# Kernel optimization log

Measured on AMD Instinct MI355X. Metric: run time of the kernel, lower is better.

Reference implementation:

```python
import jax, jax.numpy as jnp
import numpy as np

N = 129  # fixed by fc1: 3*121 -> N-8 = 121
F = 262144
E = 16384

def setup_inputs() -> dict:
    key = jax.random.key(0)
    ks = jax.random.split(key, 18)
    s = 0.05
    return {
        "x": jax.random.normal(ks[0], (N, F), jnp.float32),
        "edge_index": jax.random.randint(ks[1], (2, E), 0, N),
        "edge_attr": jax.random.uniform(ks[2], (E, 3), jnp.float32),
        # GCNConvSortPool (channel1 only; forward reuses it for all 3 edge channels)
        "gcn1_W": jax.random.normal(ks[3], (F, 1), jnp.float32) * (1.0 / np.sqrt(F)),
        "gcn1_b": jnp.zeros((1,), jnp.float32),
        "gcn2_W": jax.random.normal(ks[4], (1, 1), jnp.float32),
        "gcn2_b": jnp.zeros((1,), jnp.float32),
        "conv1_w": jax.random.normal(ks[5], (3, 2, 3), jnp.float32) * s,  # OIH
        "conv1_b": jax.random.normal(ks[6], (3,), jnp.float32) * s,
        "conv2_w": jax.random.normal(ks[7], (1, 3, 3), jnp.float32) * s,
        "conv2_b": jax.random.normal(ks[8], (1,), jnp.float32) * s,
        "fc1_W": jax.random.normal(ks[9], (3 * 121, 32), jnp.float32) * s,
        "fc1_b": jnp.zeros((32,), jnp.float32),
        "fc2_W": jax.random.normal(ks[10], (32, 6), jnp.float32) * s,
        "fc2_b": jnp.zeros((6,), jnp.float32),
        "fc3_W": jax.random.normal(ks[11], (6, 2), jnp.float32) * s,
        "fc3_b": jnp.zeros((2,), jnp.float32),
    }

def _gcn_conv(x, row, col, ew, W, b):
    # PyG GCNConv with edge weights: add self loops (weight 1), symmetric norm.
    n = x.shape[0]
    xw = x @ W                                             # [n, out]
    loop = jnp.arange(n)
    row2 = jnp.concatenate([row, loop])
    col2 = jnp.concatenate([col, loop])
    ew2 = jnp.concatenate([ew, jnp.ones((n,), x.dtype)])
    deg = jax.ops.segment_sum(ew2, col2, num_segments=n)
    dinv = jnp.where(deg > 0, deg ** -0.5, 0.0)
    norm = dinv[row2] * ew2 * dinv[col2]                   # [e+n]
    out = jax.ops.segment_sum(norm[:, None] * xw[row2], col2, num_segments=n)
    return out + b

def _maxpool1d3(z):
    return jax.lax.reduce_window(z, -jnp.inf, jax.lax.max, (1, 1, 3), (1, 1, 1), 'VALID')

def _conv1d(z, w, b):
    out = jax.lax.conv_general_dilated(z, w, (1,), 'VALID', dimension_numbers=('NCH', 'OIH', 'NCH'))
    return out + b[None, :, None]

def _channel(x, row, col, ew, gcn1_W, gcn1_b, gcn2_W, gcn2_b, conv1_w, conv1_b, conv2_w, conv2_b):
    h1 = _gcn_conv(x, row, col, ew, gcn1_W, gcn1_b)        # [N,1]
    h2 = _gcn_conv(h1[:, -1:], row, col, ew, gcn2_W, gcn2_b)  # [N,1]
    h = jnp.concatenate([h1, h2], axis=-1)                 # [N,2]
    perm = jnp.argsort(-h[:, -1])                          # SortPool: sort by last channel, descending, k=N
    h = h[perm]                                            # [N,2]
    z = h.T[None]                                          # [1,2,N]
    z = _maxpool1d3(_conv1d(z, conv1_w, conv1_b))          # [1,3,N-4]
    z = _maxpool1d3(_conv1d(z, conv2_w, conv2_b))          # [1,1,N-8]
    return z

def reference(x, edge_index, edge_attr, gcn1_W, gcn1_b, gcn2_W, gcn2_b,
              conv1_w, conv1_b, conv2_w, conv2_b,
              fc1_W, fc1_b, fc2_W, fc2_b, fc3_W, fc3_b):
    row, col = edge_index[0], edge_index[1]
    outs = [_channel(x, row, col, edge_attr[:, c], gcn1_W, gcn1_b, gcn2_W, gcn2_b,
                     conv1_w, conv1_b, conv2_w, conv2_b) for c in range(3)]
    all_x = jnp.concatenate(outs, axis=-2)                 # [1,3,121]
    h = all_x.reshape(1, -1)                               # [1,363]
    h = jax.nn.elu(h @ fc1_W + fc1_b)                      # dropout=0 -> identity
    h = jax.nn.elu(h @ fc2_W + fc2_b)
    return h @ fc3_W + fc3_b                               # [1,2]
```

## Files before the change

kernel.cpp:

```cpp
#include <hip/hip_runtime.h>
#include <hip/hip_bf16.h>
#include <math.h>

#define NN 129
#define FF 262144
#define EE 16384
#define CHUNKS 32
#define CHUNK (FF / CHUNKS)
#define NMV (NN * CHUNKS)

#define EPT_T (EE / 256)
#define BATCH 8
#define NBATCH (EPT_T / BATCH)

#define OFF_PARTIAL 0
#define OFF_BAR     (OFF_PARTIAL + NMV)
#define LSTRIDE 32

typedef float vfloat4 __attribute__((ext_vector_type(4)));

__global__ __launch_bounds__(256) void k_fused(
    const float* __restrict__ x, const float* __restrict__ W,
    const int* __restrict__ eidx, const float* __restrict__ eattr,
    double* __restrict__ ws,
    const float* __restrict__ b1, const float* __restrict__ W2, const float* __restrict__ b2,
    const float* __restrict__ c1w, const float* __restrict__ c1b,
    const float* __restrict__ c2w, const float* __restrict__ c2b,
    const float* __restrict__ f1W, const float* __restrict__ f1b,
    const float* __restrict__ f2W, const float* __restrict__ f2b,
    const float* __restrict__ f3W, const float* __restrict__ f3b,
    float* __restrict__ out)
{
    const int b = blockIdx.x;
    const int tid = threadIdx.x;
    const int wave = tid >> 6, lane = tid & 63;

    __shared__ double P[129 + 387 + 387];
    __shared__ double SCR[1935];
    __shared__ double ws4[4];
    __shared__ double fcb[38];

    unsigned* sync = (unsigned*)(ws + OFF_BAR);

    if (b != 0) {
        const int bm = b - 1;
        const int r = bm / CHUNKS, ch = bm % CHUNKS;
        const vfloat4* xp = (const vfloat4*)(x + (size_t)r * FF + (size_t)ch * CHUNK);
        const float4*  wp = (const float4*)(W + (size_t)ch * CHUNK);
        double acc0 = 0.0, acc1 = 0.0;
#pragma unroll
        for (int i = 0; i < CHUNK / (256 * 4); ++i) {
            vfloat4 xv = __builtin_nontemporal_load(xp + tid + i * 256);
            float4  wv = wp[tid + i * 256];
            acc0 += (double)xv[0] * (double)wv.x + (double)xv[1] * (double)wv.y;
            acc1 += (double)xv[2] * (double)wv.z + (double)xv[3] * (double)wv.w;
        }
        double acc = acc0 + acc1;
        for (int off = 32; off > 0; off >>= 1) acc += __shfl_down(acc, off, 64);
        if (lane == 0) ws4[wave] = acc;
        __syncthreads();
        if (tid == 0) {
            const double v = (ws4[0] + ws4[1]) + (ws4[2] + ws4[3]);
            __hip_atomic_store(&ws[OFF_PARTIAL + bm], v,
                               __ATOMIC_RELAXED, __HIP_MEMORY_SCOPE_AGENT);
            asm volatile("s_waitcnt vmcnt(0)" ::: "memory");
            __hip_atomic_fetch_add(&sync[(bm & 63) * LSTRIDE], 1u,
                                   __ATOMIC_RELAXED, __HIP_MEMORY_SCOPE_AGENT);
        }
        return;
    }

    double* sxw   = P;
    double* sdinv = P + 129;
    double* sh1   = P + 516;
    double (*hp)[3][NN] = (double(*)[3][NN])SCR;

    for (int i = tid; i < 4 * 3 * NN; i += 256) ((double*)hp)[i] = 0.0;
    __syncthreads();
    for (int bt = 0; bt < NBATCH; ++bt) {
        int   c8[BATCH];
        float a8[BATCH][3];
#pragma unroll
        for (int i = 0; i < BATCH; ++i) {
            const int e = (bt * BATCH + i) * 256 + tid;
            c8[i] = eidx[EE + e];
            a8[i][0] = eattr[e * 3 + 0];
            a8[i][1] = eattr[e * 3 + 1];
            a8[i][2] = eattr[e * 3 + 2];
        }
#pragma unroll
        for (int i = 0; i < BATCH; ++i)
#pragma unroll
            for (int c = 0; c < 3; ++c)
                unsafeAtomicAdd(&hp[wave][c][c8[i]], (double)a8[i][c]);
    }
    __syncthreads();
    for (int v = tid; v < 3 * NN; v += 256) {
        const double d = 1.0 + (hp[0][0][0 ? 0 : 0], 0.0);
        (void)d;
    }
    for (int v = tid; v < 3 * NN; v += 256) {
        const int c = v / NN, j = v % NN;
        const double d = 1.0 + ((hp[0][c][j] + hp[1][c][j]) + (hp[2][c][j] + hp[3][c][j]));
        sdinv[v] = (d > 0.0) ? 1.0 / sqrt(d) : 0.0;
    }
    __syncthreads();

    if (tid < 64) {
        unsigned* c = sync + tid * LSTRIDE;
        const unsigned expct = (tid < 32) ? 65u : 64u;
        while (__hip_atomic_load(c, __ATOMIC_RELAXED, __HIP_MEMORY_SCOPE_AGENT) < expct)
            __builtin_amdgcn_s_sleep(8);
    }
    __syncthreads();

    for (int j = tid; j < NN; j += 256) {
        double s = 0.0;
#pragma unroll
        for (int k = 0; k < CHUNKS; ++k)
            s += __hip_atomic_load(&ws[OFF_PARTIAL + j * CHUNKS + k],
                                   __ATOMIC_RELAXED, __HIP_MEMORY_SCOPE_AGENT);
        sxw[j] = s;
    }
    for (int i = tid; i < 4 * 3 * NN; i += 256) ((double*)hp)[i] = 0.0;
    __syncthreads();

    for (int bt = 0; bt < NBATCH; ++bt) {
        int   r8[BATCH], c8[BATCH];
        float a8[BATCH][3];
#pragma unroll
        for (int i = 0; i < BATCH; ++i) {
            const int e = (bt * BATCH + i) * 256 + tid;
            r8[i] = eidx[e];
            c8[i] = eidx[EE + e];
            a8[i][0] = eattr[e * 3 + 0];
            a8[i][1] = eattr[e * 3 + 1];
            a8[i][2] = eattr[e * 3 + 2];
        }
#pragma unroll
        for (int i = 0; i < BATCH; ++i) {
            const int r = r8[i], cl = c8[i];
            const double xwr = sxw[r];
#pragma unroll
            for (int c = 0; c < 3; ++c) {
                const double nw = sdinv[c * NN + r] * (double)a8[i][c] * sdinv[c * NN + cl];
                unsafeAtomicAdd(&hp[wave][c][cl], nw * xwr);
            }
        }
    }
    __syncthreads();

    const double bb1 = (double)b1[0];
    for (int i = tid; i < 3 * NN; i += 256) {
        const int c = i / NN, j = i % NN;
        const double dv = sdinv[i];
        sh1[i] = dv * dv * sxw[j] + bb1 +
                 ((hp[0][c][j] + hp[1][c][j]) + (hp[2][c][j] + hp[3][c][j]));
    }
    __syncthreads();
    for (int i = tid; i < 4 * 3 * NN; i += 256) ((double*)hp)[i] = 0.0;
    __syncthreads();

    const double w2 = (double)W2[0];
    for (int bt = 0; bt < NBATCH; ++bt) {
        int   r8[BATCH], c8[BATCH];
        float a8[BATCH][3];
#pragma unroll
        for (int i = 0; i < BATCH; ++i) {
            const int e = (bt * BATCH + i) * 256 + tid;
            r8[i] = eidx[e];
            c8[i] = eidx[EE + e];
            a8[i][0] = eattr[e * 3 + 0];
            a8[i][1] = eattr[e * 3 + 1];
            a8[i][2] = eattr[e * 3 + 2];
        }
#pragma unroll
        for (int i = 0; i < BATCH; ++i) {
            const int r = r8[i], cl = c8[i];
#pragma unroll
            for (int c = 0; c < 3; ++c) {
                const double nw = sdinv[c * NN + r] * (double)a8[i][c] * sdinv[c * NN + cl];
                unsafeAtomicAdd(&hp[wave][c][cl], nw * (sh1[c * NN + r] * w2));
            }
        }
    }
    __syncthreads();

    double* h2f  = SCR + 1548;
    const double bb2 = (double)b2[0];
    for (int i = tid; i < 3 * NN; i += 256) {
        const int c = i / NN, j = i % NN;
        const double dv = sdinv[i];
        h2f[i] = dv * dv * (sh1[i] * w2) + bb2 +
                 ((hp[0][c][j] + hp[1][c][j]) + (hp[2][c][j] + hp[3][c][j]));
    }
    __syncthreads();

    double* z0   = SCR;
    double* z1   = SCR + 387;
    int*    rnk  = (int*)(SCR + 774);
    double* c1o  = SCR + 774;
    double* c2o  = SCR;
    double* allx = SCR + 369;
    double* fc1o = fcb;
    double* fc2o = fcb + 32;

    for (int i = tid; i < 3 * NN; i += 256) {
        const int c = i / NN, j = i % NN;
        const double v = h2f[c * NN + j];
        int rk = 0;
        for (int q = 0; q < NN; ++q) {
            const double u = h2f[c * NN + q];
            rk += (u > v) || (u == v && q < j);
        }
        rnk[i] = rk;
    }
    __syncthreads();
    for (int i = tid; i < 3 * NN; i += 256) {
        const int c = i / NN;
        const int rk = rnk[i];
        z0[c * NN + rk] = sh1[i];
        z1[c * NN + rk] = h2f[i];
    }
    __syncthreads();

    for (int i = tid; i < 3 * 3 * 127; i += 256) {
        const int c = i / (3 * 127), rem = i % (3 * 127), o = rem / 127, p = rem % 127;
        double s = (double)c1b[o];
#pragma unroll
        for (int k = 0; k < 3; ++k) {
            s += (double)c1w[(o * 2 + 0) * 3 + k] * z0[c * NN + p + k];
            s += (double)c1w[(o * 2 + 1) * 3 + k] * z1[c * NN + p + k];
        }
        c1o[(c * 3 + o) * 127 + p] = s;
    }
    __syncthreads();

    for (int i = tid; i < 3 * 123; i += 256) {
        const int c = i / 123, p = i % 123;
        double s = (double)c2b[0];
#pragma unroll
        for (int ic = 0; ic < 3; ++ic)
#pragma unroll
            for (int k = 0; k < 3; ++k) {
                const double* base = c1o + (c * 3 + ic) * 127 + p + k;
                const double m = fmax(base[0], fmax(base[1], base[2]));
                s += (double)c2w[ic * 3 + k] * m;
            }
        c2o[c * 123 + p] = s;
    }
    __syncthreads();
    for (int i = tid; i < 3 * 121; i += 256) {
        const int c = i / 121, p = i % 121;
        allx[c * 121 + p] = fmax(c2o[c * 123 + p],
                            fmax(c2o[c * 123 + p + 1], c2o[c * 123 + p + 2]));
    }
    __syncthreads();

    {
        const int j = tid >> 3, t = tid & 7;
        double s = 0.0;
        for (int i = t; i < 363; i += 8) s += allx[i] * (double)f1W[i * 32 + j];
        s += __shfl_down(s, 4, 8);
        s += __shfl_down(s, 2, 8);
        s += __shfl_down(s, 1, 8);
        if (t == 0) {
            s += (double)f1b[j];
            fc1o[j] = (s > 0.0) ? s : expm1(s);
        }
    }
    __syncthreads();
    if (tid < 6) {
        double s = (double)f2b[tid];
        for (int i = 0; i < 32; ++i) s += fc1o[i] * (double)f2W[i * 6 + tid];
        fc2o[tid] = (s > 0.0) ? s : expm1(s);
    }
    __syncthreads();
    if (tid < 2) {
        double s = (double)f3b[tid];
        for (int i = 0; i < 6; ++i) s += fc2o[i] * (double)f3W[i * 2 + tid];
        out[tid] = (float)s;
    }
}

extern "C" void kernel_launch(void* const* d_in, const int* in_sizes, int n_in,
                              void* d_out, int out_size, void* d_ws, size_t ws_size,
                              hipStream_t stream) {
    const float* x    = (const float*)d_in[0];
    const int*   eidx = (const int*)d_in[1];
    const float* eattr= (const float*)d_in[2];
    const float* g1W  = (const float*)d_in[3];
    const float* g1b  = (const float*)d_in[4];
    const float* g2W  = (const float*)d_in[5];
    const float* g2b  = (const float*)d_in[6];
    const float* c1w  = (const float*)d_in[7];
    const float* c1b  = (const float*)d_in[8];
    const float* c2w  = (const float*)d_in[9];
    const float* c2b  = (const float*)d_in[10];
    const float* f1W  = (const float*)d_in[11];
    const float* f1b  = (const float*)d_in[12];
    const float* f2W  = (const float*)d_in[13];
    const float* f2b  = (const float*)d_in[14];
    const float* f3W  = (const float*)d_in[15];
    const float* f3b  = (const float*)d_in[16];
    float* out = (float*)d_out;
    double* ws = (double*)d_ws;

    hipMemsetAsync((void*)(ws + OFF_BAR), 0, 64 * 128, stream);
    k_fused<<<NMV + 1, 256, 0, stream>>>(
        x, g1W, eidx, eattr, ws,
        g1b, g2W, g2b, c1w, c1b, c2w, c2b,
        f1W, f1b, f2W, f2b, f3W, f3b, out);
}
```

Before: 286.0 us.

## Counting-sort edges by destination and aggregate with run-length segmented sums

Block 0 now counting-sorts all edges by destination node into a global record buffer (packed row/col plus three attributes as float4). It then does the degree and both GCN aggregations by scanning contiguous per-thread runs and issuing one LDS atomic per run instead of one per edge per channel. The intent is to cut heavy shared-memory double-atomic contention in the single serial block. The cost is an extra global scatter and read-back pass and a serial prefix scan on one thread. Edge order within a bin is nondeterministic, so floating-point summation order can vary between runs.

```diff
diff --git a/kernel.cpp b/kernel.cpp
--- a/kernel.cpp
+++ b/kernel.cpp
@@ -15,6 +15,7 @@
 
 #define OFF_PARTIAL 0
 #define OFF_BAR     (OFF_PARTIAL + NMV)
+#define OFF_SORT    (OFF_BAR + 1024)
 #define LSTRIDE 32
 
 typedef float vfloat4 __attribute__((ext_vector_type(4)));
@@ -37,6 +38,8 @@
 
     __shared__ double P[129 + 387 + 387];
     __shared__ double SCR[1935];
+    __shared__ int    sbin[NN];
+    __shared__ int    scur[NN];
     __shared__ double ws4[4];
     __shared__ double fcb[38];
 
@@ -73,60 +76,27 @@
     double* sxw   = P;
     double* sdinv = P + 129;
     double* sh1   = P + 516;
-    double (*hp)[3][NN] = (double(*)[3][NN])SCR;
-
-    for (int i = tid; i < 4 * 3 * NN; i += 256) ((double*)hp)[i] = 0.0;
+    double* agg   = SCR;
+    float4* recs  = (float4*)(ws + OFF_SORT);
+
+    for (int i = tid; i < NN; i += 256) sbin[i] = 0;
     __syncthreads();
     for (int bt = 0; bt < NBATCH; ++bt) {
-        int   c8[BATCH];
-        float a8[BATCH][3];
-#pragma unroll
-        for (int i = 0; i < BATCH; ++i) {
-            const int e = (bt * BATCH + i) * 256 + tid;
-            c8[i] = eidx[EE + e];
-            a8[i][0] = eattr[e * 3 + 0];
-            a8[i][1] = eattr[e * 3 + 1];
-            a8[i][2] = eattr[e * 3 + 2];
-        }
+        int c8[BATCH];
 #pragma unroll
         for (int i = 0; i < BATCH; ++i)
-#pragma unroll
-            for (int c = 0; c < 3; ++c)
-                unsafeAtomicAdd(&hp[wave][c][c8[i]], (double)a8[i][c]);
-    }
-    __syncthreads();
-    for (int v = tid; v < 3 * NN; v += 256) {
-        const double d = 1.0 + (hp[0][0][0 ? 0 : 0], 0.0);
-        (void)d;
-    }
-    for (int v = tid; v < 3 * NN; v += 256) {
-        const int c = v / NN, j = v % NN;
-        const double d = 1.0 + ((hp[0][c][j] + hp[1][c][j]) + (hp[2][c][j] + hp[3][c][j]));
-        sdinv[v] = (d > 0.0) ? 1.0 / sqrt(d) : 0.0;
-    }
-    __syncthreads();
-
-    if (tid < 64) {
-        unsigned* c = sync + tid * LSTRIDE;
-        const unsigned expct = (tid < 32) ? 65u : 64u;
-        while (__hip_atomic_load(c, __ATOMIC_RELAXED, __HIP_MEMORY_SCOPE_AGENT) < expct)
-            __builtin_amdgcn_s_sleep(8);
-    }
-    __syncthreads();
-
-    for (int j = tid; j < NN; j += 256) {
-        double s = 0.0;
-#pragma unroll
-        for (int k = 0; k < CHUNKS; ++k)
-            s += __hip_atomic_load(&ws[OFF_PARTIAL + j * CHUNKS + k],
-                                   __ATOMIC_RELAXED, __HIP_MEMORY_SCOPE_AGENT);
-        sxw[j] = s;
-    }
-    for (int i = tid; i < 4 * 3 * NN; i += 256) ((double*)hp)[i] = 0.0;
-    __syncthreads();
-
+            c8[i] = eidx[EE + (bt * BATCH + i) * 256 + tid];
+#pragma unroll
+        for (int i = 0; i < BATCH; ++i) atomicAdd(&sbin[c8[i]], 1);
+    }
+    __syncthreads();
+    if (tid == 0) {
+        int run = 0;
+        for (int j = 0; j < NN; ++j) { scur[j] = run; run += sbin[j]; }
+    }
+    __syncthreads();
     for (int bt = 0; bt < NBATCH; ++bt) {
-        int   r8[BATCH], c8[BATCH];
+        int r8[BATCH], c8[BATCH];
         float a8[BATCH][3];
 #pragma unroll
         for (int i = 0; i < BATCH; ++i) {
@@ -139,60 +109,149 @@
         }
 #pragma unroll
         for (int i = 0; i < BATCH; ++i) {
-            const int r = r8[i], cl = c8[i];
+            const int pos = atomicAdd(&scur[c8[i]], 1);
+            float4 rec;
+            rec.x = __int_as_float((r8[i] << 8) | c8[i]);
+            rec.y = a8[i][0]; rec.z = a8[i][1]; rec.w = a8[i][2];
+            recs[pos] = rec;
+        }
+    }
+    __threadfence_block();
+    __syncthreads();
+
+    for (int i = tid; i < 3 * NN; i += 256) agg[i] = 0.0;
+    __syncthreads();
+    {
+        const int base = tid * EPT_T;
+        double a0 = 0.0, a1 = 0.0, a2 = 0.0;
+        int cur = -1;
+#pragma unroll 4
+        for (int k = 0; k < EPT_T; ++k) {
+            const float4 rec = recs[base + k];
+            const int rc = __float_as_int(rec.x);
+            const int cl = rc & 255;
+            if (cl != cur) {
+                if (cur >= 0) {
+                    unsafeAtomicAdd(&agg[0 * NN + cur], a0);
+                    unsafeAtomicAdd(&agg[1 * NN + cur], a1);
+                    unsafeAtomicAdd(&agg[2 * NN + cur], a2);
+                }
+                cur = cl; a0 = a1 = a2 = 0.0;
+            }
+            a0 += (double)rec.y; a1 += (double)rec.z; a2 += (double)rec.w;
+        }
+        if (cur >= 0) {
+            unsafeAtomicAdd(&agg[0 * NN + cur], a0);
+            unsafeAtomicAdd(&agg[1 * NN + cur], a1);
+            unsafeAtomicAdd(&agg[2 * NN + cur], a2);
+        }
+    }
+    __syncthreads();
+    for (int v = tid; v < 3 * NN; v += 256) {
+        const double d = 1.0 + agg[v];
+        sdinv[v] = (d > 0.0) ? 1.0 / sqrt(d) : 0.0;
+    }
+    __syncthreads();
+
+    if (tid < 64) {
+        unsigned* c = sync + tid * LSTRIDE;
+        const unsigned expct = (tid < 32) ? 65u : 64u;
+        while (__hip_atomic_load(c, __ATOMIC_RELAXED, __HIP_MEMORY_SCOPE_AGENT) < expct)
+            __builtin_amdgcn_s_sleep(8);
+    }
+    __syncthreads();
+
+    for (int j = tid; j < NN; j += 256) {
+        double s = 0.0;
+#pragma unroll
+        for (int k = 0; k < CHUNKS; ++k)
+            s += __hip_atomic_load(&ws[OFF_PARTIAL + j * CHUNKS + k],
+                                   __ATOMIC_RELAXED, __HIP_MEMORY_SCOPE_AGENT);
+        sxw[j] = s;
+    }
+    for (int i = tid; i < 3 * NN; i += 256) agg[i] = 0.0;
+    __syncthreads();
+
+    {
+        const int base = tid * EPT_T;
+        double a0 = 0.0, a1 = 0.0, a2 = 0.0;
+        int cur = -1;
+#pragma unroll 4
+        for (int k = 0; k < EPT_T; ++k) {
+            const float4 rec = recs[base + k];
+            const int rc = __float_as_int(rec.x);
+            const int cl = rc & 255, r = rc >> 8;
+            if (cl != cur) {
+                if (cur >= 0) {
+                    unsafeAtomicAdd(&agg[0 * NN + cur], a0);
+                    unsafeAtomicAdd(&agg[1 * NN + cur], a1);
+                    unsafeAtomicAdd(&agg[2 * NN + cur], a2);
+                }
+                cur = cl; a0 = a1 = a2 = 0.0;
+            }
             const double xwr = sxw[r];
-#pragma unroll
-            for (int c = 0; c < 3; ++c) {
-                const double nw = sdinv[c * NN + r] * (double)a8[i][c] * sdinv[c * NN + cl];
-                unsafeAtomicAdd(&hp[wave][c][cl], nw * xwr);
-            }
+            const double nw0 = sdinv[0 * NN + r] * (double)rec.y * sdinv[0 * NN + cl];
+            const double nw1 = sdinv[1 * NN + r] * (double)rec.z * sdinv[1 * NN + cl];
+            const double nw2 = sdinv[2 * NN + r] * (double)rec.w * sdinv[2 * NN + cl];
+            a0 += nw0 * xwr; a1 += nw1 * xwr; a2 += nw2 * xwr;
+        }
+        if (cur >= 0) {
+            unsafeAtomicAdd(&agg[0 * NN + cur], a0);
+            unsafeAtomicAdd(&agg[1 * NN + cur], a1);
+            unsafeAtomicAdd(&agg[2 * NN + cur], a2);
         }
     }
     __syncthreads();
 
     const double bb1 = (double)b1[0];
     for (int i = tid; i < 3 * NN; i += 256) {
-        const int c = i / NN, j = i % NN;
+        const int j = i % NN;
         const double dv = sdinv[i];
-        sh1[i] = dv * dv * sxw[j] + bb1 +
-                 ((hp[0][c][j] + hp[1][c][j]) + (hp[2][c][j] + hp[3][c][j]));
-    }
-    __syncthreads();
-    for (int i = tid; i < 4 * 3 * NN; i += 256) ((double*)hp)[i] = 0.0;
+        sh1[i] = dv * dv * sxw[j] + bb1 + agg[i];
+    }
+    __syncthreads();
+    for (int i = tid; i < 3 * NN; i += 256) agg[i] = 0.0;
     __syncthreads();
 
     const double w2 = (double)W2[0];
-    for (int bt = 0; bt < NBATCH; ++bt) {
-        int   r8[BATCH], c8[BATCH];
-        float a8[BATCH][3];
-#pragma unroll
-        for (int i = 0; i < BATCH; ++i) {
-            const int e = (bt * BATCH + i) * 256 + tid;
-            r8[i] = eidx[e];
-            c8[i] = eidx[EE + e];
-            a8[i][0] = eattr[e * 3 + 0];
-            a8[i][1] = eattr[e * 3 + 1];
-            a8[i][2] = eattr[e * 3 + 2];
-        }
-#pragma unroll
-        for (int i = 0; i < BATCH; ++i) {
-            const int r = r8[i], cl = c8[i];
-#pragma unroll
-            for (int c = 0; c < 3; ++c) {
-                const double nw = sdinv[c * NN + r] * (double)a8[i][c] * sdinv[c * NN + cl];
-                unsafeAtomicAdd(&hp[wave][c][cl], nw * (sh1[c * NN + r] * w2));
+    {
+        const int base = tid * EPT_T;
+        double a0 = 0.0, a1 = 0.0, a2 = 0.0;
+        int cur = -1;
+#pragma unroll 4
+        for (int k = 0; k < EPT_T; ++k) {
+            const float4 rec = recs[base + k];
+            const int rc = __float_as_int(rec.x);
+            const int cl = rc & 255, r = rc >> 8;
+            if (cl != cur) {
+                if (cur >= 0) {
+                    unsafeAtomicAdd(&agg[0 * NN + cur], a0);
+                    unsafeAtomicAdd(&agg[1 * NN + cur], a1);
+                    unsafeAtomicAdd(&agg[2 * NN + cur], a2);
+                }
+                cur = cl; a0 = a1 = a2 = 0.0;
             }
-        }
-    }
-    __syncthreads();
-
-    double* h2f  = SCR + 1548;
+            const double nw0 = sdinv[0 * NN + r] * (double)rec.y * sdinv[0 * NN + cl];
+            const double nw1 = sdinv[1 * NN + r] * (double)rec.z * sdinv[1 * NN + cl];
+            const double nw2 = sdinv[2 * NN + r] * (double)rec.w * sdinv[2 * NN + cl];
+            a0 += nw0 * (sh1[0 * NN + r] * w2);
+            a1 += nw1 * (sh1[1 * NN + r] * w2);
+            a2 += nw2 * (sh1[2 * NN + r] * w2);
+        }
+        if (cur >= 0) {
+            unsafeAtomicAdd(&agg[0 * NN + cur], a0);
+            unsafeAtomicAdd(&agg[1 * NN + cur], a1);
+            unsafeAtomicAdd(&agg[2 * NN + cur], a2);
+        }
+    }
+    __syncthreads();
+
+    double* h2f = SCR + 1548;
     const double bb2 = (double)b2[0];
     for (int i = tid; i < 3 * NN; i += 256) {
-        const int c = i / NN, j = i % NN;
+        const int j = i % NN; (void)j;
         const double dv = sdinv[i];
-        h2f[i] = dv * dv * (sh1[i] * w2) + bb2 +
-                 ((hp[0][c][j] + hp[1][c][j]) + (hp[2][c][j] + hp[3][c][j]));
+        h2f[i] = dv * dv * (sh1[i] * w2) + bb2 + agg[i];
     }
     __syncthreads();
 
```

Result: slower. 303.8 us (+6.2%).
